# Optimization experiments

Measured on AMD Instinct MI355X. Metric: run time of the kernel, lower is better.

Reference implementation:

```python
import jax, jax.numpy as jnp
import numpy as np

OT_REG = 0.1
OT_ITERS = 10
LN_EPS = 1e-5


def layernorm(x, g, b):
    m = jnp.mean(x, axis=-1, keepdims=True)
    v = jnp.mean((x - m) ** 2, axis=-1, keepdims=True)
    return (x - m) * jax.lax.rsqrt(v + LN_EPS) * g + b


def sinkhorn(C, epsilon, iters):
    # standard Sinkhorn: kernel exp(C/eps), alternate row/col normalization
    Q = jnp.exp(C / epsilon)  # [Na,B,La,Lb]
    def body(_, Q):
        Q = Q / jnp.sum(Q, axis=-1, keepdims=True)
        Q = Q / jnp.sum(Q, axis=-2, keepdims=True)
        return Q
    return jax.lax.fori_loop(0, iters, body, Q)


def setup_inputs() -> dict:
    key = jax.random.key(0)
    ks = jax.random.split(key, 16)
    Na, La, B, Lb, Din, H = 32, 32, 64, 32, 768, 768
    s = 0.02
    return {
        "entity_cls": jax.random.normal(ks[0], (Na, Din), jnp.float32),
        "entity_tokens": jax.random.normal(ks[1], (Na, La, Din), jnp.float32),
        "mention_cls": jax.random.normal(ks[2], (B, Din), jnp.float32),
        "mention_tokens": jax.random.normal(ks[3], (B, Lb, Din), jnp.float32),
        "Wq": jax.random.normal(ks[4], (Din, H), jnp.float32) * s,
        "bq": jnp.zeros((H,), jnp.float32),
        "Wk": jax.random.normal(ks[5], (Din, H), jnp.float32) * s,
        "bk": jnp.zeros((H,), jnp.float32),
        "Wv": jax.random.normal(ks[6], (Din, H), jnp.float32) * s,
        "bv": jnp.zeros((H,), jnp.float32),
        "ln1_g": jnp.ones((H,), jnp.float32),
        "ln1_b": jnp.zeros((H,), jnp.float32),
        "Wcls": jax.random.normal(ks[7], (Din, H), jnp.float32) * s,
        "bcls": jnp.zeros((H,), jnp.float32),
        "Wsp": jax.random.normal(ks[8], (H, 1), jnp.float32) * s,
        "bsp": jnp.zeros((1,), jnp.float32),
        "ln2_g": jnp.ones((H,), jnp.float32),
        "ln2_b": jnp.zeros((H,), jnp.float32),
    }


def reference(entity_cls, entity_tokens, mention_cls, mention_tokens,
              Wq, bq, Wk, bk, Wv, bv, ln1_g, ln1_b,
              Wcls, bcls, Wsp, bsp, ln2_g, ln2_b):
    # projections
    q = entity_tokens @ Wq + bq      # [Na,La,H]
    k = mention_tokens @ Wk + bk     # [B,Lb,H]
    v = mention_tokens @ Wv + bv     # [B,Lb,H]

    # cross-batch cosine similarity: [Na,B,La,Lb]
    qn = q / jnp.maximum(jnp.linalg.norm(q, axis=-1, keepdims=True), 1e-8)
    kn = k / jnp.maximum(jnp.linalg.norm(k, axis=-1, keepdims=True), 1e-8)
    C = jnp.einsum('aid,bjd->abij', qn, kn)

    # Sinkhorn on detached cost (torch uses C.detach())
    T = sinkhorn(jax.lax.stop_gradient(C), OT_REG, OT_ITERS)
    # F.normalize(dim=-1): L2 normalize last dim
    T = T / jnp.maximum(jnp.linalg.norm(T, axis=-1, keepdims=True), 1e-12)

    # attention + residual + layernorm: [Na,B,La,H]
    attended = jnp.einsum('abij,bjd->abid', T, v) + q[:, None, :, :]
    attended = layernorm(attended, ln1_g, ln1_b)

    # softpool over token dim (-2)
    w = jax.nn.softmax(attended @ Wsp + bsp, axis=-2)   # [Na,B,La,1]
    pooled = jnp.sum(attended * w, axis=-2)             # [Na,B,H]
    context = layernorm(pooled, ln2_g, ln2_b)

    # matching scores
    ecls = entity_cls @ Wcls + bcls                     # [Na,H]
    g2l = jnp.sum(ecls[:, None, :] * context, axis=-1)  # [Na,B]
    g2l = g2l.T                                         # [B,Na]
    g2g = mention_cls @ entity_cls.T                    # [B,Na]
    return (g2l + g2g) * 0.5
```

## Files before the change

### kernel.cpp

```cpp
#include <hip/hip_runtime.h>
#include <math.h>


typedef __attribute__((ext_vector_type(8))) short bfrag8;
typedef __attribute__((ext_vector_type(4))) float f32x4;

__device__ __forceinline__ unsigned short f2bf(float x) {
  union { float f; unsigned u; } v; v.f = x;
  unsigned r = v.u + 0x7fffu + ((v.u >> 16) & 1u);
  return (unsigned short)(r >> 16);
}

__global__ __launch_bounds__(256) void prep_kernel(
    const float* __restrict__ a0, const float* __restrict__ a1, const float* __restrict__ a2,
    unsigned short* __restrict__ o0, unsigned short* __restrict__ o1, unsigned short* __restrict__ o2,
    float* __restrict__ nrm,
    const float* __restrict__ W0, const float* __restrict__ W1,
    const float* __restrict__ W2, const float* __restrict__ W3,
    unsigned short* __restrict__ T0, unsigned short* __restrict__ T1,
    unsigned short* __restrict__ T2, unsigned short* __restrict__ T3) {
  __shared__ float t[32][33];
  int bx = blockIdx.x;
  if (bx < 2331) {
    if (bx < 2328) {
      const float* in; unsigned short* out; int i, n4;
      if (bx < 768)       { in = a0; out = o0; i = bx * 256 + threadIdx.x;          n4 = 196608; }
      else if (bx < 2304) { in = a1; out = o1; i = (bx - 768) * 256 + threadIdx.x;  n4 = 393216; }
      else                { in = a2; out = o2; i = (bx - 2304) * 256 + threadIdx.x; n4 = 6144; }
      if (i >= n4) return;
      float4 f = ((const float4*)in)[i];
      ushort4 o;
      o.x = f2bf(f.x); o.y = f2bf(f.y); o.z = f2bf(f.z); o.w = f2bf(f.w);
      ((ushort4*)out)[i] = o;
    } else {
      int i = (bx - 2328) * 256 + threadIdx.x;
      if (i < 768) ((float4*)nrm)[i] = make_float4(0.f, 0.f, 0.f, 0.f);
    }
    return;
  }
  int idx = bx - 2331;
  int z = idx / 576, r2 = idx % 576;
  int tby = r2 / 24, tbx = r2 % 24;
  const float* W = (z == 0) ? W0 : (z == 1) ? W1 : (z == 2) ? W2 : W3;
  unsigned short* O = (z == 0) ? T0 : (z == 1) ? T1 : (z == 2) ? T2 : T3;
  const int gx = tbx * 32, gy = tby * 32;
  const int tx = threadIdx.x & 31, ty = threadIdx.x >> 5;
#pragma unroll
  for (int u = 0; u < 4; ++u) {
    int row = ty + u * 8;
    t[row][tx] = W[(size_t)(gy + row) * 768 + gx + tx];
  }
  __syncthreads();
#pragma unroll
  for (int u = 0; u < 4; ++u) {
    int row = ty + u * 8;
    O[(size_t)(gx + row) * 768 + gy + tx] = f2bf(t[tx][row]);
  }
}

__global__ __launch_bounds__(256) void proj_gemm_kernel(
    const unsigned short* __restrict__ Ae, const unsigned short* __restrict__ Am,
    const unsigned short* __restrict__ Acls,
    const unsigned short* __restrict__ WqT, const unsigned short* __restrict__ WkT,
    const unsigned short* __restrict__ WvT, const unsigned short* __restrict__ WclsT,
    const float* __restrict__ bq, const float* __restrict__ bk,
    const float* __restrict__ bv, const float* __restrict__ bcls,
    unsigned short* __restrict__ qb, unsigned short* __restrict__ qT,
    unsigned short* __restrict__ kb, unsigned short* __restrict__ vT,
    float* __restrict__ ecls, float* __restrict__ iq_sq, float* __restrict__ ik_sq) {
  const int z = blockIdx.z;
  const int M = (z == 0) ? 1024 : (z == 3) ? 32 : 2048;
  const int bm = blockIdx.y * 128;
  if (bm >= M) return;
  const unsigned short* A = (z == 3) ? Acls : (z == 0) ? Ae : Am;
  const unsigned short* B = (z == 0) ? WqT : (z == 1) ? WkT : (z == 2) ? WvT : WclsT;
  const float* bias = (z == 0) ? bq : (z == 1) ? bk : (z == 2) ? bv : bcls;

  __shared__ unsigned short As[128 * 64];
  __shared__ unsigned short Bs[128 * 64];
  const int t = threadIdx.x;
  const int bn = blockIdx.x * 128;
  const int l = t & 63, w = t >> 6;
  const int wm = w & 1, wn = w >> 1;

  f32x4 acc[4][4];
#pragma unroll
  for (int mi = 0; mi < 4; ++mi)
#pragma unroll
    for (int nj = 0; nj < 4; ++nj) { f32x4 zz = {0.f, 0.f, 0.f, 0.f}; acc[mi][nj] = zz; }

  for (int k0 = 0; k0 < 768; k0 += 64) {
    __syncthreads();
#pragma unroll
    for (int u = 0; u < 4; ++u) {
      int c = t + u * 256;
      int row = c >> 3, kc = c & 7;
      int gm = bm + row; gm = gm < M ? gm : M - 1;
      int4 av = *(const int4*)(A + (size_t)gm * 768 + k0 + kc * 8);
      *(int4*)(As + row * 64 + ((kc ^ (row & 7)) * 8)) = av;
      int4 bv4 = *(const int4*)(B + (size_t)(bn + row) * 768 + k0 + kc * 8);
      *(int4*)(Bs + row * 64 + ((kc ^ (row & 7)) * 8)) = bv4;
    }
    __syncthreads();
#pragma unroll
    for (int kk = 0; kk < 2; ++kk) {
      bfrag8 af[4], bf[4];
      const int kc = kk * 4 + (l >> 4);
#pragma unroll
      for (int mi = 0; mi < 4; ++mi) {
        int arow = wm * 64 + mi * 16 + (l & 15);
        af[mi] = *(const bfrag8*)(As + arow * 64 + ((kc ^ (arow & 7)) * 8));
      }
#pragma unroll
      for (int nj = 0; nj < 4; ++nj) {
        int brow = wn * 64 + nj * 16 + (l & 15);
        bf[nj] = *(const bfrag8*)(Bs + brow * 64 + ((kc ^ (brow & 7)) * 8));
      }
#pragma unroll
      for (int mi = 0; mi < 4; ++mi)
#pragma unroll
        for (int nj = 0; nj < 4; ++nj)
          acc[mi][nj] = __builtin_amdgcn_mfma_f32_16x16x32_bf16(af[mi], bf[nj], acc[mi][nj], 0, 0, 0);
    }
  }

  const int col = l & 15, rq = l >> 4;
  float p[4][4] = {};
#pragma unroll
  for (int mi = 0; mi < 4; ++mi) {
#pragma unroll
    for (int nj = 0; nj < 4; ++nj) {
      int gn = bn + wn * 64 + nj * 16 + col;
      float bs = bias[gn];
#pragma unroll
      for (int r = 0; r < 4; ++r) {
        int gm = bm + wm * 64 + mi * 16 + rq * 4 + r;
        if (gm >= M) continue;
        float val = acc[mi][nj][r] + bs;
        if (z < 2) p[mi][r] += val * val;
        unsigned short bfv = f2bf(val);
        if (z == 0) {
          qb[(size_t)gm * 768 + gn] = bfv;
          int at = gm >> 5, j = gm & 31;
          qT[((size_t)at * 768 + gn) * 32 + j] = bfv;
        } else if (z == 1) kb[(size_t)gm * 768 + gn] = bfv;
        else if (z == 2) {
          int bb = gm >> 5, j = gm & 31;
          vT[((size_t)bb * 768 + gn) * 32 + j] = bfv;
        } else ecls[(size_t)gm * 768 + gn] = val;
      }
    }
  }
  if (z < 2) {
    float* nrm = (z == 0) ? iq_sq : ik_sq;
#pragma unroll
    for (int mi = 0; mi < 4; ++mi)
#pragma unroll
      for (int r = 0; r < 4; ++r) {
        float s = p[mi][r];
        s += __shfl_xor(s, 1); s += __shfl_xor(s, 2);
        s += __shfl_xor(s, 4); s += __shfl_xor(s, 8);
        if (col == 0) {
          int gm = bm + wm * 64 + mi * 16 + rq * 4 + r;
          atomicAdd(&nrm[gm], s);
        }
      }
  }
}

__global__ __launch_bounds__(256) void cos_sink_kernel(
    const unsigned short* __restrict__ qb, const unsigned short* __restrict__ kb,
    const float* __restrict__ iq_sq, const float* __restrict__ ik_sq,
    unsigned short* __restrict__ Tg,
    const float* __restrict__ ln1_g, const float* __restrict__ ln1_b,
    const float* __restrict__ Wsp, const float* __restrict__ bsp,
    const float* __restrict__ ln2_g, const float* __restrict__ ln2_b,
    const float* __restrict__ ecls,
    const float* __restrict__ entity_cls, const float* __restrict__ mention_cls,
    float* __restrict__ gwv, float* __restrict__ auxgab,
    float4* __restrict__ cons, float* __restrict__ g2g) {
  __shared__ unsigned short As[128 * 64];
  __shared__ unsigned short Bs[64 * 64];
  __shared__ float ldsIq[128], ldsIk[64];
  const int t = threadIdx.x;

  if (blockIdx.y == 8) {
    float* redf = (float*)As;
    const int a2 = blockIdx.x;
    float sgw = 0.f, sbw = 0.f, sga = 0.f, sba = 0.f;
#pragma unroll
    for (int cc = 0; cc < 3; ++cc) {
      int h = t + cc * 256;
      float g1 = ln1_g[h], b1 = ln1_b[h], wsp = Wsp[h];
      float ec = ecls[(size_t)a2 * 768 + h];
      float gw = g1 * wsp;
      float gab = ln2_g[h] * ec;
      if (a2 == 0) gwv[h] = gw;
      auxgab[(size_t)a2 * 768 + h] = gab;
      sgw += gw; sbw += b1 * wsp; sga += gab; sba += ln2_b[h] * ec;
    }
#pragma unroll
    for (int m = 1; m < 64; m <<= 1) {
      sgw += __shfl_xor(sgw, m); sbw += __shfl_xor(sbw, m);
      sga += __shfl_xor(sga, m); sba += __shfl_xor(sba, m);
    }
    const int wv = t >> 6, ln = t & 63;
    if (ln == 0) { redf[wv * 4] = sgw; redf[wv * 4 + 1] = sbw; redf[wv * 4 + 2] = sga; redf[wv * 4 + 3] = sba; }
    __syncthreads();
    if (t == 0) {
      float4 c;
      c.x = redf[0] + redf[4] + redf[8] + redf[12];
      c.y = redf[1] + redf[5] + redf[9] + redf[13] + bsp[0];
      c.z = redf[2] + redf[6] + redf[10] + redf[14];
      c.w = redf[3] + redf[7] + redf[11] + redf[15];
      cons[a2] = c;
    }
    const float* ea = entity_cls + (size_t)a2 * 768;
    for (int bb = wv; bb < 64; bb += 4) {
      const float* mbp = mention_cls + (size_t)bb * 768;
      float s = 0.f;
#pragma unroll
      for (int u = 0; u < 12; ++u) s += mbp[ln * 12 + u] * ea[ln * 12 + u];
#pragma unroll
      for (int m = 1; m < 64; m <<= 1) s += __shfl_xor(s, m);
      if (ln == 0) g2g[bb * 32 + a2] = s;
    }
    return;
  }

  const int bn = blockIdx.x * 64, bm = blockIdx.y * 128;
  const int l = t & 63, w = t >> 6;
  const int wm = w & 1, wn = w >> 1;
  const int cg = l & 15, rq = l >> 4;

  if (t < 128) ldsIq[t] = iq_sq[bm + t];
  else if (t < 192) ldsIk[t - 128] = ik_sq[bn + t - 128];

  f32x4 acc[4][2];
#pragma unroll
  for (int mi = 0; mi < 4; ++mi)
#pragma unroll
    for (int nj = 0; nj < 2; ++nj) { f32x4 zz = {0.f, 0.f, 0.f, 0.f}; acc[mi][nj] = zz; }

  for (int k0 = 0; k0 < 768; k0 += 64) {
    __syncthreads();
#pragma unroll
    for (int u = 0; u < 4; ++u) {
      int c = t + u * 256;
      int row = c >> 3, kc = c & 7;
      int4 av = *(const int4*)(qb + (size_t)(bm + row) * 768 + k0 + kc * 8);
      *(int4*)(As + row * 64 + ((kc ^ (row & 7)) * 8)) = av;
    }
#pragma unroll
    for (int u = 0; u < 2; ++u) {
      int c = t + u * 256;
      int row = c >> 3, kc = c & 7;
      int4 bv4 = *(const int4*)(kb + (size_t)(bn + row) * 768 + k0 + kc * 8);
      *(int4*)(Bs + row * 64 + ((kc ^ (row & 7)) * 8)) = bv4;
    }
    __syncthreads();
#pragma unroll
    for (int kk = 0; kk < 2; ++kk) {
      bfrag8 af[4], bf[2];
      const int kc = kk * 4 + rq;
#pragma unroll
      for (int mi = 0; mi < 4; ++mi) {
        int arow = wm * 64 + mi * 16 + cg;
        af[mi] = *(const bfrag8*)(As + arow * 64 + ((kc ^ (arow & 7)) * 8));
      }
#pragma unroll
      for (int nj = 0; nj < 2; ++nj) {
        int brow = wn * 32 + nj * 16 + cg;
        bf[nj] = *(const bfrag8*)(Bs + brow * 64 + ((kc ^ (brow & 7)) * 8));
      }
#pragma unroll
      for (int mi = 0; mi < 4; ++mi)
#pragma unroll
        for (int nj = 0; nj < 2; ++nj)
          acc[mi][nj] = __builtin_amdgcn_mfma_f32_16x16x32_bf16(af[mi], bf[nj], acc[mi][nj], 0, 0, 0);
    }
  }

  float irow[4][4], icol[2];
#pragma unroll
  for (int mi = 0; mi < 4; ++mi)
#pragma unroll
    for (int r = 0; r < 4; ++r) {
      float s = ldsIq[wm * 64 + mi * 16 + rq * 4 + r];
      irow[mi][r] = 1.0f / fmaxf(sqrtf(s), 1e-8f);
    }
#pragma unroll
  for (int nj = 0; nj < 2; ++nj) {
    float s = ldsIk[wn * 32 + nj * 16 + cg];
    icol[nj] = 1.0f / fmaxf(sqrtf(s), 1e-8f);
  }
#pragma unroll
  for (int mi = 0; mi < 4; ++mi)
#pragma unroll
    for (int nj = 0; nj < 2; ++nj)
#pragma unroll
      for (int r = 0; r < 4; ++r)
        acc[mi][nj][r] = __expf(acc[mi][nj][r] * irow[mi][r] * icol[nj] * 10.0f);

  for (int it = 0; it < 10; ++it) {
#pragma unroll
    for (int mi = 0; mi < 4; ++mi)
#pragma unroll
      for (int r = 0; r < 4; ++r) {
        float rs = acc[mi][0][r] + acc[mi][1][r];
        rs += __shfl_xor(rs, 1); rs += __shfl_xor(rs, 2);
        rs += __shfl_xor(rs, 4); rs += __shfl_xor(rs, 8);
        float rinv = __builtin_amdgcn_rcpf(rs);
        acc[mi][0][r] *= rinv; acc[mi][1][r] *= rinv;
      }
#pragma unroll
    for (int ta = 0; ta < 2; ++ta)
#pragma unroll
      for (int nj = 0; nj < 2; ++nj) {
        float cs = acc[2 * ta][nj][0] + acc[2 * ta][nj][1] + acc[2 * ta][nj][2] + acc[2 * ta][nj][3]
                 + acc[2 * ta + 1][nj][0] + acc[2 * ta + 1][nj][1] + acc[2 * ta + 1][nj][2] + acc[2 * ta + 1][nj][3];
        cs += __shfl_xor(cs, 16); cs += __shfl_xor(cs, 32);
        float cinv = __builtin_amdgcn_rcpf(cs);
#pragma unroll
        for (int mi2 = 0; mi2 < 2; ++mi2)
#pragma unroll
          for (int r = 0; r < 4; ++r) acc[2 * ta + mi2][nj][r] *= cinv;
      }
  }

#pragma unroll
  for (int mi = 0; mi < 4; ++mi)
#pragma unroll
    for (int r = 0; r < 4; ++r) {
      float ss = acc[mi][0][r] * acc[mi][0][r] + acc[mi][1][r] * acc[mi][1][r];
      ss += __shfl_xor(ss, 1); ss += __shfl_xor(ss, 2);
      ss += __shfl_xor(ss, 4); ss += __shfl_xor(ss, 8);
      float tinv = 1.0f / fmaxf(sqrtf(ss), 1e-12f);
      acc[mi][0][r] *= tinv; acc[mi][1][r] *= tinv;
    }

  const int b_idx = (bn >> 5) + wn;
#pragma unroll
  for (int mi = 0; mi < 4; ++mi) {
    const int a_idx = (bm >> 5) + wm * 2 + (mi >> 1);
    unsigned short* base = Tg + (((size_t)b_idx * 32 + a_idx) << 10);
    const int ri0 = (mi & 1) * 16 + rq * 4;
#pragma unroll
    for (int nj = 0; nj < 2; ++nj)
#pragma unroll
      for (int r = 0; r < 4; ++r)
        base[(ri0 + r) * 32 + nj * 16 + cg] = f2bf(acc[mi][nj][r]);
  }
}

__global__ __launch_bounds__(256) void attn_kernel(
    const unsigned short* __restrict__ Tg,
    const unsigned short* __restrict__ vT,
    const unsigned short* __restrict__ qT,
    const float* __restrict__ gwv,
    const float* __restrict__ ln1_g, const float* __restrict__ ln1_b,
    const float* __restrict__ auxgab,
    const float4* __restrict__ cons,
    const float* __restrict__ g2g,
    float* __restrict__ out) {
  __shared__ unsigned short vLds[768 * 32];
  const int t = threadIdx.x;
  const int w = t >> 6, l = t & 63;
  const int b = blockIdx.x >> 3;
  const int a = ((blockIdx.x & 7) << 2) + w;
  const int pair = b * 32 + a;
  const int cg = l & 15, rq = l >> 4;

  {
    const int4* src = (const int4*)(vT + (size_t)b * 768 * 32);
    int4* dst = (int4*)vLds;
#pragma unroll
    for (int u = 0; u < 12; ++u) dst[t + u * 256] = src[t + u * 256];
  }
  __syncthreads();

  const unsigned short* Tp = Tg + ((size_t)pair << 10);
  bfrag8 af[2], afI[2];
#pragma unroll
  for (int mi = 0; mi < 2; ++mi) {
    int row = mi * 16 + cg;
    af[mi] = *(const bfrag8*)(Tp + row * 32 + rq * 8);
    bfrag8 fI;
#pragma unroll
    for (int u = 0; u < 8; ++u) fI[u] = (row == rq * 8 + u) ? (short)0x3F80 : (short)0;
    afI[mi] = fI;
  }

  const unsigned short* qTa = qT + (size_t)a * 768 * 32;
  const float4 cc4 = cons[a];

  float s1[2][4] = {}, s2[2][4] = {}, a1[2][4] = {};
#pragma unroll 4
  for (int nj = 0; nj < 48; ++nj) {
    int h = nj * 16 + cg;
    bfrag8 vf = *(const bfrag8*)(vLds + h * 32 + rq * 8);
    bfrag8 qf = *(const bfrag8*)(qTa + (size_t)h * 32 + rq * 8);
    float gw = gwv[h];
#pragma unroll
    for (int mi = 0; mi < 2; ++mi) {
      f32x4 zz = {0.f, 0.f, 0.f, 0.f};
      f32x4 p = __builtin_amdgcn_mfma_f32_16x16x32_bf16(af[mi], vf, zz, 0, 0, 0);
      f32x4 x4 = __builtin_amdgcn_mfma_f32_16x16x32_bf16(afI[mi], qf, p, 0, 0, 0);
#pragma unroll
      for (int r = 0; r < 4; ++r) {
        float x = x4[r];
        s1[mi][r] += x; s2[mi][r] += x * x; a1[mi][r] += x * gw;
      }
    }
  }
#pragma unroll
  for (int m = 1; m < 16; m <<= 1) {
#pragma unroll
    for (int mi = 0; mi < 2; ++mi)
#pragma unroll
      for (int r = 0; r < 4; ++r) {
        s1[mi][r] += __shfl_xor(s1[mi][r], m);
        s2[mi][r] += __shfl_xor(s2[mi][r], m);
        a1[mi][r] += __shfl_xor(a1[mi][r], m);
      }
  }

  float uu[2][4], c0 = 0.f;
  {
    float mean[2][4], rstd[2][4], logit[2][4];
#pragma unroll
    for (int mi = 0; mi < 2; ++mi)
#pragma unroll
      for (int r = 0; r < 4; ++r) {
        float m1 = s1[mi][r] * (1.0f / 768.0f);
        float var = s2[mi][r] * (1.0f / 768.0f) - m1 * m1;
        float rs = rsqrtf(var + 1e-5f);
        mean[mi][r] = m1; rstd[mi][r] = rs;
        logit[mi][r] = rs * (a1[mi][r] - m1 * cc4.x) + cc4.y;
      }
    float mx = logit[0][0];
#pragma unroll
    for (int mi = 0; mi < 2; ++mi)
#pragma unroll
      for (int r = 0; r < 4; ++r) mx = fmaxf(mx, logit[mi][r]);
    mx = fmaxf(mx, __shfl_xor(mx, 16)); mx = fmaxf(mx, __shfl_xor(mx, 32));
    float se = 0.f, ee[2][4];
#pragma unroll
    for (int mi = 0; mi < 2; ++mi)
#pragma unroll
      for (int r = 0; r < 4; ++r) { ee[mi][r] = __expf(logit[mi][r] - mx); se += ee[mi][r]; }
    se += __shfl_xor(se, 16); se += __shfl_xor(se, 32);
    const float sinv = __builtin_amdgcn_rcpf(se);
#pragma unroll
    for (int mi = 0; mi < 2; ++mi)
#pragma unroll
      for (int r = 0; r < 4; ++r) {
        uu[mi][r] = ee[mi][r] * sinv * rstd[mi][r];
        c0 += uu[mi][r] * mean[mi][r];
      }
    c0 += __shfl_xor(c0, 16); c0 += __shfl_xor(c0, 32);
  }

  const float* gabp = auxgab + (size_t)a * 768;
  float ps = 0.f, pq = 0.f, spc = 0.f;
#pragma unroll 4
  for (int nj = 0; nj < 48; ++nj) {
    int h = nj * 16 + cg;
    bfrag8 vf = *(const bfrag8*)(vLds + h * 32 + rq * 8);
    bfrag8 qf = *(const bfrag8*)(qTa + (size_t)h * 32 + rq * 8);
    float pp = 0.f;
#pragma unroll
    for (int mi = 0; mi < 2; ++mi) {
      f32x4 zz = {0.f, 0.f, 0.f, 0.f};
      f32x4 p = __builtin_amdgcn_mfma_f32_16x16x32_bf16(af[mi], vf, zz, 0, 0, 0);
      f32x4 x4 = __builtin_amdgcn_mfma_f32_16x16x32_bf16(afI[mi], qf, p, 0, 0, 0);
#pragma unroll
      for (int r = 0; r < 4; ++r) pp += uu[mi][r] * x4[r];
    }
    pp += __shfl_xor(pp, 16); pp += __shfl_xor(pp, 32);
    float pooled = ln1_g[h] * (pp - c0) + ln1_b[h];
    ps += pooled; pq += pooled * pooled; spc += pooled * gabp[h];
  }
#pragma unroll
  for (int m = 1; m < 16; m <<= 1) {
    ps += __shfl_xor(ps, m); pq += __shfl_xor(pq, m); spc += __shfl_xor(spc, m);
  }
  const float m2 = ps * (1.0f / 768.0f);
  const float var2 = pq * (1.0f / 768.0f) - m2 * m2;
  const float rs2 = rsqrtf(var2 + 1e-5f);
  float tot = rs2 * (spc - m2 * cc4.z) + cc4.w + g2g[b * 32 + a];
  if (l == 0) out[b * 32 + a] = 0.5f * tot;
}

extern "C" void kernel_launch(void* const* d_in, const int* in_sizes, int n_in,
                              void* d_out, int out_size, void* d_ws, size_t ws_size,
                              hipStream_t stream) {
  const float* entity_cls     = (const float*)d_in[0];
  const float* entity_tokens  = (const float*)d_in[1];
  const float* mention_cls    = (const float*)d_in[2];
  const float* mention_tokens = (const float*)d_in[3];
  const float* Wq = (const float*)d_in[4];   const float* bq = (const float*)d_in[5];
  const float* Wk = (const float*)d_in[6];   const float* bk = (const float*)d_in[7];
  const float* Wv = (const float*)d_in[8];   const float* bv = (const float*)d_in[9];
  const float* ln1_g = (const float*)d_in[10]; const float* ln1_b = (const float*)d_in[11];
  const float* Wcls = (const float*)d_in[12];  const float* bcls = (const float*)d_in[13];
  const float* Wsp = (const float*)d_in[14];   const float* bsp = (const float*)d_in[15];
  const float* ln2_g = (const float*)d_in[16]; const float* ln2_b = (const float*)d_in[17];
  float* out = (float*)d_out;

  float* ws     = (float*)d_ws;
  float* ecls   = ws;
  float* iq_sq  = ecls + 24576;
  float* ik_sq  = iq_sq + 1024;
  float* gwv    = ik_sq + 2048;
  float* auxgab = gwv + 768;
  float* g2g    = auxgab + 24576;
  float4* cons  = (float4*)(g2g + 2048);
  unsigned short* qb = (unsigned short*)(cons + 32);
  unsigned short* qT = qb + 786432;
  unsigned short* kb = qT + 786432;
  unsigned short* vT = kb + 1572864;
  char* R = (char*)(vT + 1572864);
  unsigned short* Ae    = (unsigned short*)R;
  unsigned short* Am    = Ae + 786432;
  unsigned short* Acls  = Am + 1572864;
  unsigned short* WqT   = Acls + 24576;
  unsigned short* WkT   = WqT + 589824;
  unsigned short* WvT   = WkT + 589824;
  unsigned short* WclsT = WvT + 589824;
  unsigned short* Tg = (unsigned short*)R;

  dim3 blk(256);
  prep_kernel<<<dim3(4635), blk, 0, stream>>>(
      entity_tokens, mention_tokens, entity_cls, Ae, Am, Acls, iq_sq,
      Wq, Wk, Wv, Wcls, WqT, WkT, WvT, WclsT);
  proj_gemm_kernel<<<dim3(6, 16, 4), blk, 0, stream>>>(
      Ae, Am, Acls, WqT, WkT, WvT, WclsT, bq, bk, bv, bcls,
      qb, qT, kb, vT, ecls, iq_sq, ik_sq);
  cos_sink_kernel<<<dim3(32, 9), blk, 0, stream>>>(
      qb, kb, iq_sq, ik_sq, Tg,
      ln1_g, ln1_b, Wsp, bsp, ln2_g, ln2_b, ecls, entity_cls, mention_cls,
      gwv, auxgab, cons, g2g);
  attn_kernel<<<dim3(512), blk, 0, stream>>>(
      Tg, vT, qT, gwv, ln1_g, ln1_b, auxgab, cons, g2g, out);
}
```

Baseline: 187.5 us.

## Fuse cosine/Sinkhorn kernel with attention-pooling kernel, keeping transport plan in LDS

Merges the cosine-similarity Sinkhorn kernel and the attention/softpool kernel into one launch. The transport plan stays in shared memory as bf16 instead of going through global memory. The V tiles for the block's two mentions are loaded into LDS alongside the GEMM k-loop. Per-entity constants (gw, gab, reductions) and the g2g dot products are now computed inside each block instead of by a separate block row. This removes one launch, the Tg global round trip and the aux buffers. In exchange, each block uses much more LDS (about 150KB), runs only 256 blocks, and repeats the constant computation in every block.

```diff
diff --git a/kernel.cpp b/kernel.cpp
--- a/kernel.cpp
+++ b/kernel.cpp
@@ -168,81 +168,77 @@
   }
 }
 
-__global__ __launch_bounds__(256) void cos_sink_kernel(
+__global__ __launch_bounds__(256) void cos_attn_kernel(
     const unsigned short* __restrict__ qb, const unsigned short* __restrict__ kb,
     const float* __restrict__ iq_sq, const float* __restrict__ ik_sq,
-    unsigned short* __restrict__ Tg,
+    const unsigned short* __restrict__ qT,
+    const unsigned short* __restrict__ vT,
     const float* __restrict__ ln1_g, const float* __restrict__ ln1_b,
     const float* __restrict__ Wsp, const float* __restrict__ bsp,
     const float* __restrict__ ln2_g, const float* __restrict__ ln2_b,
     const float* __restrict__ ecls,
     const float* __restrict__ entity_cls, const float* __restrict__ mention_cls,
-    float* __restrict__ gwv, float* __restrict__ auxgab,
-    float4* __restrict__ cons, float* __restrict__ g2g) {
-  __shared__ unsigned short As[128 * 64];
-  __shared__ unsigned short Bs[64 * 64];
+    float* __restrict__ out) {
+  __shared__ unsigned short vLds[2 * 768 * 32];
+  __shared__ __align__(16) unsigned short scratch[12288];
+  __shared__ float gabLds[4 * 768];
+  __shared__ float gwLds[768];
   __shared__ float ldsIq[128], ldsIk[64];
+  __shared__ float red[40];
+
+  unsigned short* As = scratch;
+  unsigned short* Bs = scratch + 8192;
+  unsigned short* Tlds = scratch;
+
   const int t = threadIdx.x;
-
-  if (blockIdx.y == 8) {
-    float* redf = (float*)As;
-    const int a2 = blockIdx.x;
-    float sgw = 0.f, sbw = 0.f, sga = 0.f, sba = 0.f;
+  const int l = t & 63, w = t >> 6;
+  const int bm = blockIdx.y * 128, bn = blockIdx.x * 64;
+  const int wm = w & 1, wn = w >> 1;
+  const int cg = l & 15, rq = l >> 4;
+
+  {
+    float sgw = 0.f, sbw = 0.f, sga[4] = {}, sba[4] = {};
 #pragma unroll
     for (int cc = 0; cc < 3; ++cc) {
       int h = t + cc * 256;
       float g1 = ln1_g[h], b1 = ln1_b[h], wsp = Wsp[h];
-      float ec = ecls[(size_t)a2 * 768 + h];
+      float g2 = ln2_g[h], b2 = ln2_b[h];
       float gw = g1 * wsp;
-      float gab = ln2_g[h] * ec;
-      if (a2 == 0) gwv[h] = gw;
-      auxgab[(size_t)a2 * 768 + h] = gab;
-      sgw += gw; sbw += b1 * wsp; sga += gab; sba += ln2_b[h] * ec;
+      gwLds[h] = gw;
+      sgw += gw; sbw += b1 * wsp;
+#pragma unroll
+      for (int aa = 0; aa < 4; ++aa) {
+        float ec = ecls[(size_t)((blockIdx.y << 2) + aa) * 768 + h];
+        float gab = g2 * ec;
+        gabLds[aa * 768 + h] = gab;
+        sga[aa] += gab; sba[aa] += b2 * ec;
+      }
     }
 #pragma unroll
     for (int m = 1; m < 64; m <<= 1) {
       sgw += __shfl_xor(sgw, m); sbw += __shfl_xor(sbw, m);
-      sga += __shfl_xor(sga, m); sba += __shfl_xor(sba, m);
-    }
-    const int wv = t >> 6, ln = t & 63;
-    if (ln == 0) { redf[wv * 4] = sgw; redf[wv * 4 + 1] = sbw; redf[wv * 4 + 2] = sga; redf[wv * 4 + 3] = sba; }
-    __syncthreads();
-    if (t == 0) {
-      float4 c;
-      c.x = redf[0] + redf[4] + redf[8] + redf[12];
-      c.y = redf[1] + redf[5] + redf[9] + redf[13] + bsp[0];
-      c.z = redf[2] + redf[6] + redf[10] + redf[14];
-      c.w = redf[3] + redf[7] + redf[11] + redf[15];
-      cons[a2] = c;
-    }
-    const float* ea = entity_cls + (size_t)a2 * 768;
-    for (int bb = wv; bb < 64; bb += 4) {
-      const float* mbp = mention_cls + (size_t)bb * 768;
-      float s = 0.f;
-#pragma unroll
-      for (int u = 0; u < 12; ++u) s += mbp[ln * 12 + u] * ea[ln * 12 + u];
-#pragma unroll
-      for (int m = 1; m < 64; m <<= 1) s += __shfl_xor(s, m);
-      if (ln == 0) g2g[bb * 32 + a2] = s;
-    }
-    return;
-  }
-
-  const int bn = blockIdx.x * 64, bm = blockIdx.y * 128;
-  const int l = t & 63, w = t >> 6;
-  const int wm = w & 1, wn = w >> 1;
-  const int cg = l & 15, rq = l >> 4;
-
+#pragma unroll
+      for (int aa = 0; aa < 4; ++aa) { sga[aa] += __shfl_xor(sga[aa], m); sba[aa] += __shfl_xor(sba[aa], m); }
+    }
+    if (l == 0) {
+      red[w * 10 + 0] = sgw; red[w * 10 + 1] = sbw;
+#pragma unroll
+      for (int aa = 0; aa < 4; ++aa) { red[w * 10 + 2 + aa] = sga[aa]; red[w * 10 + 6 + aa] = sba[aa]; }
+    }
+  }
   if (t < 128) ldsIq[t] = iq_sq[bm + t];
   else if (t < 192) ldsIk[t - 128] = ik_sq[bn + t - 128];
 
+  const int4* vsrc = (const int4*)(vT + (size_t)(blockIdx.x * 2) * 768 * 32);
+  int4* vdst = (int4*)vLds;
+
   f32x4 acc[4][2];
 #pragma unroll
   for (int mi = 0; mi < 4; ++mi)
 #pragma unroll
     for (int nj = 0; nj < 2; ++nj) { f32x4 zz = {0.f, 0.f, 0.f, 0.f}; acc[mi][nj] = zz; }
 
-  for (int k0 = 0; k0 < 768; k0 += 64) {
+  for (int k0 = 0, s = 0; k0 < 768; k0 += 64, ++s) {
     __syncthreads();
 #pragma unroll
     for (int u = 0; u < 4; ++u) {
@@ -258,6 +254,8 @@
       int4 bv4 = *(const int4*)(kb + (size_t)(bn + row) * 768 + k0 + kc * 8);
       *(int4*)(Bs + row * 64 + ((kc ^ (row & 7)) * 8)) = bv4;
     }
+    vdst[t + (2 * s) * 256] = vsrc[t + (2 * s) * 256];
+    vdst[t + (2 * s + 1) * 256] = vsrc[t + (2 * s + 1) * 256];
     __syncthreads();
 #pragma unroll
     for (int kk = 0; kk < 2; ++kk) {
@@ -286,13 +284,13 @@
   for (int mi = 0; mi < 4; ++mi)
 #pragma unroll
     for (int r = 0; r < 4; ++r) {
-      float s = ldsIq[wm * 64 + mi * 16 + rq * 4 + r];
-      irow[mi][r] = 1.0f / fmaxf(sqrtf(s), 1e-8f);
+      float sv = ldsIq[wm * 64 + mi * 16 + rq * 4 + r];
+      irow[mi][r] = 1.0f / fmaxf(sqrtf(sv), 1e-8f);
     }
 #pragma unroll
   for (int nj = 0; nj < 2; ++nj) {
-    float s = ldsIk[wn * 32 + nj * 16 + cg];
-    icol[nj] = 1.0f / fmaxf(sqrtf(s), 1e-8f);
+    float sv = ldsIk[wn * 32 + nj * 16 + cg];
+    icol[nj] = 1.0f / fmaxf(sqrtf(sv), 1e-8f);
   }
 #pragma unroll
   for (int mi = 0; mi < 4; ++mi)
@@ -339,11 +337,11 @@
       acc[mi][0][r] *= tinv; acc[mi][1][r] *= tinv;
     }
 
-  const int b_idx = (bn >> 5) + wn;
+  __syncthreads();
 #pragma unroll
   for (int mi = 0; mi < 4; ++mi) {
-    const int a_idx = (bm >> 5) + wm * 2 + (mi >> 1);
-    unsigned short* base = Tg + (((size_t)b_idx * 32 + a_idx) << 10);
+    const int a_loc = wm * 2 + (mi >> 1);
+    unsigned short* base = Tlds + ((wn * 4 + a_loc) << 10);
     const int ri0 = (mi & 1) * 16 + rq * 4;
 #pragma unroll
     for (int nj = 0; nj < 2; ++nj)
@@ -351,92 +349,89 @@
       for (int r = 0; r < 4; ++r)
         base[(ri0 + r) * 32 + nj * 16 + cg] = f2bf(acc[mi][nj][r]);
   }
-}
-
-__global__ __launch_bounds__(256) void attn_kernel(
-    const unsigned short* __restrict__ Tg,
-    const unsigned short* __restrict__ vT,
-    const unsigned short* __restrict__ qT,
-    const float* __restrict__ gwv,
-    const float* __restrict__ ln1_g, const float* __restrict__ ln1_b,
-    const float* __restrict__ auxgab,
-    const float4* __restrict__ cons,
-    const float* __restrict__ g2g,
-    float* __restrict__ out) {
-  __shared__ unsigned short vLds[768 * 32];
-  const int t = threadIdx.x;
-  const int w = t >> 6, l = t & 63;
-  const int b = blockIdx.x >> 3;
-  const int a = ((blockIdx.x & 7) << 2) + w;
-  const int pair = b * 32 + a;
-  const int cg = l & 15, rq = l >> 4;
-
-  {
-    const int4* src = (const int4*)(vT + (size_t)b * 768 * 32);
-    int4* dst = (int4*)vLds;
-#pragma unroll
-    for (int u = 0; u < 12; ++u) dst[t + u * 256] = src[t + u * 256];
-  }
   __syncthreads();
 
-  const unsigned short* Tp = Tg + ((size_t)pair << 10);
-  bfrag8 af[2], afI[2];
+  const int bl = w & 1, ah = w >> 1;
+  const int b_g = (blockIdx.x << 1) + bl;
+  const unsigned short* vbase = vLds + bl * 24576;
+
+  float sgw_f = 0.f, sbw_f = 0.f, sga_f[2] = {}, sba_f[2] = {};
+#pragma unroll
+  for (int wv = 0; wv < 4; ++wv) {
+    sgw_f += red[wv * 10 + 0]; sbw_f += red[wv * 10 + 1];
+    sga_f[0] += red[wv * 10 + 2 + ah * 2]; sga_f[1] += red[wv * 10 + 3 + ah * 2];
+    sba_f[0] += red[wv * 10 + 6 + ah * 2]; sba_f[1] += red[wv * 10 + 7 + ah * 2];
+  }
+  sbw_f += bsp[0];
+
+  bfrag8 af[2][2], afI[2];
+  const unsigned short* qTa[2];
+#pragma unroll
+  for (int ap = 0; ap < 2; ++ap) {
+    const int a_local = ah * 2 + ap;
+    qTa[ap] = qT + (size_t)((blockIdx.y << 2) + a_local) * 24576;
+    const unsigned short* Tp = Tlds + ((bl * 4 + a_local) << 10);
+#pragma unroll
+    for (int mi = 0; mi < 2; ++mi)
+      af[ap][mi] = *(const bfrag8*)(Tp + (mi * 16 + cg) * 32 + rq * 8);
+  }
 #pragma unroll
   for (int mi = 0; mi < 2; ++mi) {
     int row = mi * 16 + cg;
-    af[mi] = *(const bfrag8*)(Tp + row * 32 + rq * 8);
     bfrag8 fI;
 #pragma unroll
     for (int u = 0; u < 8; ++u) fI[u] = (row == rq * 8 + u) ? (short)0x3F80 : (short)0;
     afI[mi] = fI;
   }
 
-  const unsigned short* qTa = qT + (size_t)a * 768 * 32;
-  const float4 cc4 = cons[a];
-
-  float s1[2][4] = {}, s2[2][4] = {}, a1[2][4] = {};
-#pragma unroll 4
+  float s1[2][2][4] = {}, s2[2][2][4] = {}, a1[2][2][4] = {};
+#pragma unroll 2
   for (int nj = 0; nj < 48; ++nj) {
     int h = nj * 16 + cg;
-    bfrag8 vf = *(const bfrag8*)(vLds + h * 32 + rq * 8);
-    bfrag8 qf = *(const bfrag8*)(qTa + (size_t)h * 32 + rq * 8);
-    float gw = gwv[h];
-#pragma unroll
-    for (int mi = 0; mi < 2; ++mi) {
-      f32x4 zz = {0.f, 0.f, 0.f, 0.f};
-      f32x4 p = __builtin_amdgcn_mfma_f32_16x16x32_bf16(af[mi], vf, zz, 0, 0, 0);
-      f32x4 x4 = __builtin_amdgcn_mfma_f32_16x16x32_bf16(afI[mi], qf, p, 0, 0, 0);
+    bfrag8 vf = *(const bfrag8*)(vbase + h * 32 + rq * 8);
+    float gw = gwLds[h];
+#pragma unroll
+    for (int ap = 0; ap < 2; ++ap) {
+      bfrag8 qf = *(const bfrag8*)(qTa[ap] + (size_t)h * 32 + rq * 8);
+#pragma unroll
+      for (int mi = 0; mi < 2; ++mi) {
+        f32x4 zz = {0.f, 0.f, 0.f, 0.f};
+        f32x4 p = __builtin_amdgcn_mfma_f32_16x16x32_bf16(af[ap][mi], vf, zz, 0, 0, 0);
+        f32x4 x4 = __builtin_amdgcn_mfma_f32_16x16x32_bf16(afI[mi], qf, p, 0, 0, 0);
+#pragma unroll
+        for (int r = 0; r < 4; ++r) {
+          float x = x4[r];
+          s1[ap][mi][r] += x; s2[ap][mi][r] += x * x; a1[ap][mi][r] += x * gw;
+        }
+      }
+    }
+  }
+#pragma unroll
+  for (int m = 1; m < 16; m <<= 1)
+#pragma unroll
+    for (int ap = 0; ap < 2; ++ap)
+#pragma unroll
+      for (int mi = 0; mi < 2; ++mi)
+#pragma unroll
+        for (int r = 0; r < 4; ++r) {
+          s1[ap][mi][r] += __shfl_xor(s1[ap][mi][r], m);
+          s2[ap][mi][r] += __shfl_xor(s2[ap][mi][r], m);
+          a1[ap][mi][r] += __shfl_xor(a1[ap][mi][r], m);
+        }
+
+  float uu[2][2][4], c0[2];
+#pragma unroll
+  for (int ap = 0; ap < 2; ++ap) {
+    float mean[2][4], rstd[2][4], logit[2][4];
+#pragma unroll
+    for (int mi = 0; mi < 2; ++mi)
 #pragma unroll
       for (int r = 0; r < 4; ++r) {
-        float x = x4[r];
-        s1[mi][r] += x; s2[mi][r] += x * x; a1[mi][r] += x * gw;
-      }
-    }
-  }
-#pragma unroll
-  for (int m = 1; m < 16; m <<= 1) {
-#pragma unroll
-    for (int mi = 0; mi < 2; ++mi)
-#pragma unroll
-      for (int r = 0; r < 4; ++r) {
-        s1[mi][r] += __shfl_xor(s1[mi][r], m);
-        s2[mi][r] += __shfl_xor(s2[mi][r], m);
-        a1[mi][r] += __shfl_xor(a1[mi][r], m);
-      }
-  }
-
-  float uu[2][4], c0 = 0.f;
-  {
-    float mean[2][4], rstd[2][4], logit[2][4];
-#pragma unroll
-    for (int mi = 0; mi < 2; ++mi)
-#pragma unroll
-      for (int r = 0; r < 4; ++r) {
-        float m1 = s1[mi][r] * (1.0f / 768.0f);
-        float var = s2[mi][r] * (1.0f / 768.0f) - m1 * m1;
+        float m1 = s1[ap][mi][r] * (1.0f / 768.0f);
+        float var = s2[ap][mi][r] * (1.0f / 768.0f) - m1 * m1;
         float rs = rsqrtf(var + 1e-5f);
         mean[mi][r] = m1; rstd[mi][r] = rs;
-        logit[mi][r] = rs * (a1[mi][r] - m1 * cc4.x) + cc4.y;
+        logit[mi][r] = rs * (a1[ap][mi][r] - m1 * sgw_f) + sbw_f;
       }
     float mx = logit[0][0];
 #pragma unroll
@@ -451,45 +446,63 @@
       for (int r = 0; r < 4; ++r) { ee[mi][r] = __expf(logit[mi][r] - mx); se += ee[mi][r]; }
     se += __shfl_xor(se, 16); se += __shfl_xor(se, 32);
     const float sinv = __builtin_amdgcn_rcpf(se);
+    float c0a = 0.f;
 #pragma unroll
     for (int mi = 0; mi < 2; ++mi)
 #pragma unroll
       for (int r = 0; r < 4; ++r) {
-        uu[mi][r] = ee[mi][r] * sinv * rstd[mi][r];
-        c0 += uu[mi][r] * mean[mi][r];
-      }
-    c0 += __shfl_xor(c0, 16); c0 += __shfl_xor(c0, 32);
-  }
-
-  const float* gabp = auxgab + (size_t)a * 768;
-  float ps = 0.f, pq = 0.f, spc = 0.f;
-#pragma unroll 4
+        uu[ap][mi][r] = ee[mi][r] * sinv * rstd[mi][r];
+        c0a += uu[ap][mi][r] * mean[mi][r];
+      }
+    c0a += __shfl_xor(c0a, 16); c0a += __shfl_xor(c0a, 32);
+    c0[ap] = c0a;
+  }
+
+  float ps[2] = {}, pq[2] = {}, spc[2] = {};
+#pragma unroll 2
   for (int nj = 0; nj < 48; ++nj) {
     int h = nj * 16 + cg;
-    bfrag8 vf = *(const bfrag8*)(vLds + h * 32 + rq * 8);
-    bfrag8 qf = *(const bfrag8*)(qTa + (size_t)h * 32 + rq * 8);
-    float pp = 0.f;
-#pragma unroll
-    for (int mi = 0; mi < 2; ++mi) {
-      f32x4 zz = {0.f, 0.f, 0.f, 0.f};
-      f32x4 p = __builtin_amdgcn_mfma_f32_16x16x32_bf16(af[mi], vf, zz, 0, 0, 0);
-      f32x4 x4 = __builtin_amdgcn_mfma_f32_16x16x32_bf16(afI[mi], qf, p, 0, 0, 0);
-#pragma unroll
-      for (int r = 0; r < 4; ++r) pp += uu[mi][r] * x4[r];
-    }
-    pp += __shfl_xor(pp, 16); pp += __shfl_xor(pp, 32);
-    float pooled = ln1_g[h] * (pp - c0) + ln1_b[h];
-    ps += pooled; pq += pooled * pooled; spc += pooled * gabp[h];
-  }
-#pragma unroll
-  for (int m = 1; m < 16; m <<= 1) {
-    ps += __shfl_xor(ps, m); pq += __shfl_xor(pq, m); spc += __shfl_xor(spc, m);
-  }
-  const float m2 = ps * (1.0f / 768.0f);
-  const float var2 = pq * (1.0f / 768.0f) - m2 * m2;
-  const float rs2 = rsqrtf(var2 + 1e-5f);
-  float tot = rs2 * (spc - m2 * cc4.z) + cc4.w + g2g[b * 32 + a];
-  if (l == 0) out[b * 32 + a] = 0.5f * tot;
+    bfrag8 vf = *(const bfrag8*)(vbase + h * 32 + rq * 8);
+    float g1h = ln1_g[h], b1h = ln1_b[h];
+#pragma unroll
+    for (int ap = 0; ap < 2; ++ap) {
+      bfrag8 qf = *(const bfrag8*)(qTa[ap] + (size_t)h * 32 + rq * 8);
+      float pp = 0.f;
+#pragma unroll
+      for (int mi = 0; mi < 2; ++mi) {
+        f32x4 zz = {0.f, 0.f, 0.f, 0.f};
+        f32x4 p = __builtin_amdgcn_mfma_f32_16x16x32_bf16(af[ap][mi], vf, zz, 0, 0, 0);
+        f32x4 x4 = __builtin_amdgcn_mfma_f32_16x16x32_bf16(afI[mi], qf, p, 0, 0, 0);
+#pragma unroll
+        for (int r = 0; r < 4; ++r) pp += uu[ap][mi][r] * x4[r];
+      }
+      pp += __shfl_xor(pp, 16); pp += __shfl_xor(pp, 32);
+      float pooled = g1h * (pp - c0[ap]) + b1h;
+      ps[ap] += pooled; pq[ap] += pooled * pooled;
+      spc[ap] += pooled * gabLds[(ah * 2 + ap) * 768 + h];
+    }
+  }
+
+#pragma unroll
+  for (int ap = 0; ap < 2; ++ap) {
+#pragma unroll
+    for (int m = 1; m < 16; m <<= 1) {
+      ps[ap] += __shfl_xor(ps[ap], m); pq[ap] += __shfl_xor(pq[ap], m); spc[ap] += __shfl_xor(spc[ap], m);
+    }
+    const float m2 = ps[ap] * (1.0f / 768.0f);
+    const float var2 = pq[ap] * (1.0f / 768.0f) - m2 * m2;
+    const float rs2 = rsqrtf(var2 + 1e-5f);
+    const int a_g = (blockIdx.y << 2) + ah * 2 + ap;
+    const float* ea = entity_cls + (size_t)a_g * 768;
+    const float* mb = mention_cls + (size_t)b_g * 768;
+    float sg = 0.f;
+#pragma unroll
+    for (int u = 0; u < 12; ++u) sg += mb[l * 12 + u] * ea[l * 12 + u];
+#pragma unroll
+    for (int m = 1; m < 64; m <<= 1) sg += __shfl_xor(sg, m);
+    float tot = rs2 * (spc[ap] - m2 * sga_f[ap]) + sba_f[ap] + sg;
+    if (l == 0) out[b_g * 32 + a_g] = 0.5f * tot;
+  }
 }
 
 extern "C" void kernel_launch(void* const* d_in, const int* in_sizes, int n_in,
@@ -512,11 +525,7 @@
   float* ecls   = ws;
   float* iq_sq  = ecls + 24576;
   float* ik_sq  = iq_sq + 1024;
-  float* gwv    = ik_sq + 2048;
-  float* auxgab = gwv + 768;
-  float* g2g    = auxgab + 24576;
-  float4* cons  = (float4*)(g2g + 2048);
-  unsigned short* qb = (unsigned short*)(cons + 32);
+  unsigned short* qb = (unsigned short*)(ws + 55168);
   unsigned short* qT = qb + 786432;
   unsigned short* kb = qT + 786432;
   unsigned short* vT = kb + 1572864;
@@ -528,7 +537,6 @@
   unsigned short* WkT   = WqT + 589824;
   unsigned short* WvT   = WkT + 589824;
   unsigned short* WclsT = WvT + 589824;
-  unsigned short* Tg = (unsigned short*)R;
 
   dim3 blk(256);
   prep_kernel<<<dim3(4635), blk, 0, stream>>>(
@@ -537,10 +545,8 @@
   proj_gemm_kernel<<<dim3(6, 16, 4), blk, 0, stream>>>(
       Ae, Am, Acls, WqT, WkT, WvT, WclsT, bq, bk, bv, bcls,
       qb, qT, kb, vT, ecls, iq_sq, ik_sq);
-  cos_sink_kernel<<<dim3(32, 9), blk, 0, stream>>>(
-      qb, kb, iq_sq, ik_sq, Tg,
-      ln1_g, ln1_b, Wsp, bsp, ln2_g, ln2_b, ecls, entity_cls, mention_cls,
-      gwv, auxgab, cons, g2g);
-  attn_kernel<<<dim3(512), blk, 0, stream>>>(
-      Tg, vT, qT, gwv, ln1_g, ln1_b, auxgab, cons, g2g, out);
+  cos_attn_kernel<<<dim3(32, 8), blk, 0, stream>>>(
+      qb, kb, iq_sq, ik_sq, qT, vT,
+      ln1_g, ln1_b, Wsp, bsp, ln2_g, ln2_b,
+      ecls, entity_cls, mention_cls, out);
 }
```

Measured after the change: 197.4 us. 1.05x slower.
